# Kernel tuning notes

Measured on AMD Instinct MI355X. Metric: run time of the kernel, lower is better.

## Reference

```python
import jax, jax.numpy as jnp
import numpy as np

B, S, D = 2, 2048, 1024
H, A = 16, 64  # num_heads, attention_dim


def setup_inputs() -> dict:
    key = jax.random.key(0)
    ks = jax.random.split(key, 9)
    sd = D ** -0.5
    so = (H * A) ** -0.5
    return {
        "x": jax.random.normal(ks[0], (B, S, D), dtype=jnp.float32),
        "Wq": jax.random.normal(ks[1], (D, H * A), dtype=jnp.float32) * sd,
        "bq": jnp.zeros((H * A,), dtype=jnp.float32),
        "Wk": jax.random.normal(ks[2], (D, H * A), dtype=jnp.float32) * sd,
        "bk": jnp.zeros((H * A,), dtype=jnp.float32),
        "Wv": jax.random.normal(ks[3], (D, H * A), dtype=jnp.float32) * sd,
        "bv": jnp.zeros((H * A,), dtype=jnp.float32),
        "Wo": jax.random.normal(ks[4], (H * A, D), dtype=jnp.float32) * so,
        "bo": jnp.zeros((D,), dtype=jnp.float32),
    }


def reference(x, Wq, bq, Wk, bk, Wv, bv, Wo, bo):
    b, s, _ = x.shape
    # project and split heads: [b, s, H, A]
    q = (x @ Wq + bq).reshape(b, s, H, A)
    k = (x @ Wk + bk).reshape(b, s, H, A)
    v = (x @ Wv + bv).reshape(b, s, H, A)
    # scores [b, H, s, s]
    scores = jnp.einsum("bqhd,bkhd->bhqk", q, k) / jnp.sqrt(jnp.float32(A))
    weights = jax.nn.softmax(scores, axis=-1)
    attended = jnp.einsum("bhqk,bkhd->bqhd", weights, v).reshape(b, s, H * A)
    return attended @ Wo + bo
```

## Files before the change

### kernel.cpp

```cpp
#include <hip/hip_runtime.h>
#include <hip/hip_bf16.h>

typedef __attribute__((ext_vector_type(8))) short bf16x8;
typedef __attribute__((ext_vector_type(4))) float f32x4;

#define LOG2E 1.44269504088896f

extern "C" __device__ float __ocml_native_exp2_f32(float);

__device__ __forceinline__ unsigned short f2bf(float f) {
    union { float f; unsigned int u; } v; v.f = f;
    unsigned int r = v.u + 0x7FFF + ((v.u >> 16) & 1);
    return (unsigned short)(r >> 16);
}

__device__ __forceinline__ unsigned int pk_bf16(float lo, float hi) {
    unsigned int r;
    asm("v_cvt_pk_bf16_f32 %0, %1, %2" : "=v"(r) : "v"(lo), "v"(hi));
    return r;
}

typedef __attribute__((address_space(3))) unsigned int lds_uint;
typedef __attribute__((address_space(1))) const unsigned int glob_uint;
__device__ __forceinline__ void gl2lds16(const void* g, void* l) {
    __builtin_amdgcn_global_load_lds((glob_uint*)g, (lds_uint*)l, 16, 0, 0);
}

__global__ __launch_bounds__(256) void cvt_bf16(const float* __restrict__ in,
                                                unsigned int* __restrict__ out, int n4) {
    int i = blockIdx.x * 256 + threadIdx.x;
    if (i >= n4) return;
    float4 v = ((const float4*)in)[i];
    uint2 o;
    o.x = pk_bf16(v.x, v.y);
    o.y = pk_bf16(v.z, v.w);
    ((uint2*)out)[i] = o;
}

__global__ __launch_bounds__(256) void transpose4_bf16(
    const float* __restrict__ w0, const float* __restrict__ w1,
    const float* __restrict__ w2, const float* __restrict__ w3,
    unsigned short* __restrict__ o0, unsigned short* __restrict__ o1,
    unsigned short* __restrict__ o2, unsigned short* __restrict__ o3) {
    const int z = blockIdx.z;
    const float* in = (z == 0) ? w0 : (z == 1) ? w1 : (z == 2) ? w2 : w3;
    unsigned short* out = (z == 0) ? o0 : (z == 1) ? o1 : (z == 2) ? o2 : o3;
    __shared__ float t[32][33];
    int tx = threadIdx.x & 31, ty = threadIdx.x >> 5;
    int r0 = blockIdx.y * 32, c0 = blockIdx.x * 32;
    for (int i = 0; i < 32; i += 8)
        t[ty + i][tx] = in[(size_t)(r0 + ty + i) * 1024 + c0 + tx];
    __syncthreads();
    for (int i = 0; i < 32; i += 8)
        out[(size_t)(c0 + ty + i) * 1024 + r0 + tx] = f2bf(t[tx][ty + i]);
}

__device__ __forceinline__ void gemm_core(const short* __restrict__ A,
                                          const short* __restrict__ BT,
                                          int K, int bm0, int bn0,
                                          short* As, short* Bs, f32x4 acc[4][4]) {
    const int tid = threadIdx.x;
    const int lane = tid & 63;
    const int w = tid >> 6;
    const int wr0 = (w >> 1) * 64;
    const int wc0 = (w & 1) * 64;
    const int l15 = lane & 15, quad = lane >> 4;
    const int sr = lane >> 2;
    const int slog = (lane & 3) ^ (sr & 3);

    for (int i = 0; i < 4; i++)
        for (int j = 0; j < 4; j++) acc[i][j] = (f32x4)0.f;

    for (int k0 = 0; k0 < K; k0 += 32) {
        for (int i = 0; i < 4; i++) {
            int c = w * 4 + i;
            if (c < 8)
                gl2lds16(A + (size_t)(bm0 + c * 16 + sr) * K + k0 + slog * 8,
                         As + c * 512);
            else
                gl2lds16(BT + (size_t)(bn0 + (c - 8) * 16 + sr) * K + k0 + slog * 8,
                         Bs + (c - 8) * 512);
        }
        __syncthreads();
        const int ph = (quad ^ (l15 & 3)) * 8;
        bf16x8 af[4], bfr[4];
        for (int im = 0; im < 4; im++)
            af[im] = *(const bf16x8*)&As[(wr0 + im * 16 + l15) * 32 + ph];
        for (int in = 0; in < 4; in++)
            bfr[in] = *(const bf16x8*)&Bs[(wc0 + in * 16 + l15) * 32 + ph];
        for (int im = 0; im < 4; im++)
            for (int in = 0; in < 4; in++)
                acc[im][in] = __builtin_amdgcn_mfma_f32_16x16x32_bf16(af[im], bfr[in], acc[im][in], 0, 0, 0);
        __syncthreads();
    }
}

__global__ __launch_bounds__(256) void gemm_qkv(
    const short* __restrict__ xb,
    const short* __restrict__ wqT, const short* __restrict__ wkT, const short* __restrict__ wvT,
    const float* __restrict__ bq, const float* __restrict__ bk, const float* __restrict__ bv,
    unsigned short* __restrict__ qb, unsigned short* __restrict__ kb, unsigned short* __restrict__ vTb) {
    __shared__ short As[4096], Bs[4096];
    const int z = blockIdx.z;
    const short* Amat = (z == 2) ? wvT : xb;
    const short* Bmat = (z == 0) ? wqT : (z == 1) ? wkT : xb;
    const float* bias = (z == 0) ? bq : (z == 1) ? bk : bv;
    const float scl = (z == 0) ? 0.125f * LOG2E : 1.f;
    const int bm0 = (z == 2) ? blockIdx.y * 128 : blockIdx.x * 128;
    const int bn0 = (z == 2) ? blockIdx.x * 128 : blockIdx.y * 128;
    f32x4 acc[4][4];
    gemm_core(Amat, Bmat, 1024, bm0, bn0, As, Bs, acc);
    const int lane = threadIdx.x & 63, w = threadIdx.x >> 6;
    const int wr0 = (w >> 1) * 64, wc0 = (w & 1) * 64, l15 = lane & 15, quad = lane >> 4;
    if (z == 2) {
        for (int im = 0; im < 4; im++)
            for (int in = 0; in < 4; in++)
                for (int r = 0; r < 4; r++) {
                    int rowa = bm0 + wr0 + im * 16 + quad * 4 + r;
                    int colg = bn0 + wc0 + in * 16 + l15;
                    unsigned short ov = f2bf(acc[im][in][r] + bias[rowa]);
                    int b = colg >> 11, s = colg & 2047;
                    vTb[(size_t)b * 2097152 + (size_t)rowa * 2048 + s] = ov;
                }
    } else {
        for (int im = 0; im < 4; im++)
            for (int in = 0; in < 4; in++)
                for (int r = 0; r < 4; r++) {
                    int rowg = bm0 + wr0 + im * 16 + quad * 4 + r;
                    int colg = bn0 + wc0 + in * 16 + l15;
                    unsigned short ov = f2bf((acc[im][in][r] + bias[colg]) * scl);
                    int b = rowg >> 11, s = rowg & 2047;
                    int h = colg >> 6, a = colg & 63;
                    int bh = b * 16 + h;
                    if (z == 0) qb[((size_t)bh * 2048 + s) * 64 + a] = ov;
                    else        kb[((size_t)bh * 2048 + s) * 64 + a] = ov;
                }
    }
}

__global__ __launch_bounds__(512, 2) void gemm_out(
    const short* __restrict__ att, const short* __restrict__ woT,
    const float* __restrict__ bo, float* __restrict__ out) {
    __shared__ short As[4096], Bs[4096];
    const int bm0 = blockIdx.x * 128, bn0 = blockIdx.y * 128;
    const int tid = threadIdx.x, lane = tid & 63, w = tid >> 6;
    const int wr0 = (w >> 1) * 32, wc0 = (w & 1) * 64;
    const int l15 = lane & 15, quad = lane >> 4;
    const int sr = lane >> 2;
    const int slog = (lane & 3) ^ (sr & 3);

    f32x4 acc[2][4];
    for (int i = 0; i < 2; i++)
        for (int j = 0; j < 4; j++) acc[i][j] = (f32x4)0.f;

    for (int k0 = 0; k0 < 1024; k0 += 32) {
        for (int i = 0; i < 2; i++) {
            int c = w * 2 + i;
            if (c < 8)
                gl2lds16(att + (size_t)(bm0 + c * 16 + sr) * 1024 + k0 + slog * 8,
                         As + c * 512);
            else
                gl2lds16(woT + (size_t)(bn0 + (c - 8) * 16 + sr) * 1024 + k0 + slog * 8,
                         Bs + (c - 8) * 512);
        }
        __syncthreads();
        const int ph = (quad ^ (l15 & 3)) * 8;
        bf16x8 af[2], bfr[4];
        for (int im = 0; im < 2; im++)
            af[im] = *(const bf16x8*)&As[(wr0 + im * 16 + l15) * 32 + ph];
        for (int in = 0; in < 4; in++)
            bfr[in] = *(const bf16x8*)&Bs[(wc0 + in * 16 + l15) * 32 + ph];
        for (int im = 0; im < 2; im++)
            for (int in = 0; in < 4; in++)
                acc[im][in] = __builtin_amdgcn_mfma_f32_16x16x32_bf16(af[im], bfr[in], acc[im][in], 0, 0, 0);
        __syncthreads();
    }
    for (int im = 0; im < 2; im++)
        for (int in = 0; in < 4; in++)
            for (int r = 0; r < 4; r++) {
                int rowg = bm0 + wr0 + im * 16 + quad * 4 + r;
                int colg = bn0 + wc0 + in * 16 + l15;
                out[(size_t)rowg * 1024 + colg] = acc[im][in][r] + bo[colg];
            }
}

__global__ __launch_bounds__(256, 2) void flash_attn(
    const unsigned short* __restrict__ qb, const unsigned short* __restrict__ kb,
    const unsigned short* __restrict__ vTb, unsigned short* __restrict__ att) {
    __shared__ short QP[9216];
    __shared__ short Ks[2][4096];
    __shared__ short Vs[2][4096];
    const int tid = threadIdx.x, lane = tid & 63, w = tid >> 6;
    const int l15 = lane & 15, quad = lane >> 4;
    const int q0 = blockIdx.x * 128;
    const int bh = blockIdx.y;
    const size_t qkbase = (size_t)bh * 2048 * 64;
    const size_t vbase = (size_t)bh * 64 * 2048;
    const int sr = lane >> 3;
    const int slog = (lane & 7) ^ sr;
    const int l7 = l15 & 7;

    for (int i = 0; i < 8; i++) {
        int c = w * 8 + i;
        if (c < 16)
            gl2lds16(qb + qkbase + (size_t)(q0 + c * 8 + sr) * 64 + slog * 8, QP + c * 512);
        else if (c < 24)
            gl2lds16(kb + qkbase + (size_t)((c - 16) * 8 + sr) * 64 + slog * 8,
                     Ks[0] + (c - 16) * 512);
        else
            gl2lds16(vTb + vbase + (size_t)((c - 24) * 8 + sr) * 2048 + slog * 8,
                     Vs[0] + (c - 24) * 512);
    }
    __syncthreads();

    const int wq0 = w * 32;
    const int c0 = (quad ^ l7) * 8, c1 = c0 ^ 32;
    const int fb = l15 * 64;
    bf16x8 aqA0 = *(const bf16x8*)&QP[(wq0 + l15) * 64 + c0];
    bf16x8 aqB0 = *(const bf16x8*)&QP[(wq0 + l15) * 64 + c1];
    bf16x8 aqA1 = *(const bf16x8*)&QP[(wq0 + 16 + l15) * 64 + c0];
    bf16x8 aqB1 = *(const bf16x8*)&QP[(wq0 + 16 + l15) * 64 + c1];
    __syncthreads();

    f32x4 o[4][2];
    for (int dt = 0; dt < 4; dt++)
        for (int rt = 0; rt < 2; rt++) o[dt][rt] = (f32x4)0.f;
    f32x4 ls0 = (f32x4)0.f, ls1 = (f32x4)0.f;

    short* Pw = QP + w * 2304;
    short* Pst = Pw + l15 * 72 + quad * 4;
    const short* Prd = Pw + l15 * 72 + quad * 8;

    const unsigned short* sgp;
    int sgcall, sgtile;
    short *sb0, *sb1;
    if (w < 2) {
        sgp = kb + qkbase + (size_t)(64 + w * 32 + sr) * 64 + slog * 8;
        sgcall = 512;
        sgtile = 4096;
        sb0 = Ks[0] + w * 2048; sb1 = Ks[1] + w * 2048;
    } else {
        sgp = vTb + vbase + (size_t)((w - 2) * 32 + sr) * 2048 + 64 + slog * 8;
        sgcall = 16384;
        sgtile = 64;
        sb0 = Vs[0] + (w - 2) * 2048; sb1 = Vs[1] + (w - 2) * 2048;
    }

    auto step = [&](const short* Kb, const short* Vb, bool stage,
                    const unsigned short* sg, short* sd) {
        if (stage) {
#pragma unroll
            for (int i = 0; i < 4; i++)
                gl2lds16(sg + (size_t)i * sgcall, sd + i * 512);
        }
        f32x4 sc[4][2];
#pragma unroll
        for (int t = 0; t < 4; t++) {
            bf16x8 ak = *(const bf16x8*)(Kb + fb + c0 + t * 1024);
            sc[t][0] = __builtin_amdgcn_mfma_f32_16x16x32_bf16(ak, aqA0, (f32x4)0.f, 0, 0, 0);
            sc[t][1] = __builtin_amdgcn_mfma_f32_16x16x32_bf16(ak, aqA1, (f32x4)0.f, 0, 0, 0);
        }
#pragma unroll
        for (int t = 0; t < 4; t++) {
            bf16x8 ak = *(const bf16x8*)(Kb + fb + c1 + t * 1024);
            sc[t][0] = __builtin_amdgcn_mfma_f32_16x16x32_bf16(ak, aqB0, sc[t][0], 0, 0, 0);
            sc[t][1] = __builtin_amdgcn_mfma_f32_16x16x32_bf16(ak, aqB1, sc[t][1], 0, 0, 0);
        }
#pragma unroll
        for (int t = 0; t < 4; t++) {
#pragma unroll
            for (int r = 0; r < 4; r++) {
                sc[t][0][r] = __ocml_native_exp2_f32(sc[t][0][r]);
                sc[t][1][r] = __ocml_native_exp2_f32(sc[t][1][r]);
            }
            ls0 += sc[t][0];
            ls1 += sc[t][1];
            uint2 pk0, pk1;
            pk0.x = pk_bf16(sc[t][0][0], sc[t][0][1]);
            pk0.y = pk_bf16(sc[t][0][2], sc[t][0][3]);
            pk1.x = pk_bf16(sc[t][1][0], sc[t][1][1]);
            pk1.y = pk_bf16(sc[t][1][2], sc[t][1][3]);
            *(uint2*)(Pst + t * 16) = pk0;
            *(uint2*)(Pst + 1152 + t * 16) = pk1;
        }
#pragma unroll
        for (int t2 = 0; t2 < 2; t2++) {
            bf16x8 bp0 = *(const bf16x8*)(Prd + t2 * 32);
            bf16x8 bp1 = *(const bf16x8*)(Prd + 1152 + t2 * 32);
            const int cc = t2 ? c1 : c0;
#pragma unroll
            for (int dt = 0; dt < 4; dt++) {
                bf16x8 av = *(const bf16x8*)(Vb + fb + cc + dt * 1024);
                o[dt][0] = __builtin_amdgcn_mfma_f32_16x16x32_bf16(av, bp0, o[dt][0], 0, 0, 0);
                o[dt][1] = __builtin_amdgcn_mfma_f32_16x16x32_bf16(av, bp1, o[dt][1], 0, 0, 0);
            }
        }
        __syncthreads();
    };

    for (int kv0 = 0; kv0 < 2048; kv0 += 128) {
        step(Ks[0], Vs[0], true, sgp, sb1);
        sgp += sgtile;
        step(Ks[1], Vs[1], kv0 + 128 < 2048, sgp, sb0);
        sgp += sgtile;
    }

    const int b = bh >> 4, h = bh & 15;
#pragma unroll
    for (int rt = 0; rt < 2; rt++) {
        f32x4 ls = rt ? ls1 : ls0;
        float l = (ls[0] + ls[1]) + (ls[2] + ls[3]);
        l += __shfl_xor(l, 16);
        l += __shfl_xor(l, 32);
        float inv = 1.f / l;
        int s = q0 + wq0 + rt * 16 + l15;
        for (int dt = 0; dt < 4; dt++) {
            uint2 pk;
            pk.x = pk_bf16(o[dt][rt][0] * inv, o[dt][rt][1] * inv);
            pk.y = pk_bf16(o[dt][rt][2] * inv, o[dt][rt][3] * inv);
            int col = h * 64 + dt * 16 + quad * 4;
            *(uint2*)&att[((size_t)b * 2048 + s) * 1024 + col] = pk;
        }
    }
}

extern "C" void kernel_launch(void* const* d_in, const int* in_sizes, int n_in,
                              void* d_out, int out_size, void* d_ws, size_t ws_size,
                              hipStream_t stream) {
    const float* x  = (const float*)d_in[0];
    const float* Wq = (const float*)d_in[1];
    const float* bq = (const float*)d_in[2];
    const float* Wk = (const float*)d_in[3];
    const float* bk = (const float*)d_in[4];
    const float* Wv = (const float*)d_in[5];
    const float* bv = (const float*)d_in[6];
    const float* Wo = (const float*)d_in[7];
    const float* bo = (const float*)d_in[8];
    float* out = (float*)d_out;

    short* ws  = (short*)d_ws;
    short* xb  = ws;
    short* wqT = ws + 4 * 1024 * 1024;
    short* wkT = wqT + 1024 * 1024;
    short* wvT = wkT + 1024 * 1024;
    short* woT = wvT + 1024 * 1024;
    short* qb  = woT + 1024 * 1024;
    short* kb  = qb + 4 * 1024 * 1024;
    short* vTb = kb + 4 * 1024 * 1024;
    short* att = vTb + 4 * 1024 * 1024;

    cvt_bf16<<<4096, 256, 0, stream>>>(x, (unsigned int*)xb, 1024 * 1024);
    transpose4_bf16<<<dim3(32, 32, 4), 256, 0, stream>>>(
        Wq, Wk, Wv, Wo,
        (unsigned short*)wqT, (unsigned short*)wkT,
        (unsigned short*)wvT, (unsigned short*)woT);
    gemm_qkv<<<dim3(32, 8, 3), 256, 0, stream>>>(xb, wqT, wkT, wvT, bq, bk, bv,
                                                 (unsigned short*)qb, (unsigned short*)kb,
                                                 (unsigned short*)vTb);
    flash_attn<<<dim3(16, 32), 256, 0, stream>>>((const unsigned short*)qb,
                                                 (const unsigned short*)kb,
                                                 (const unsigned short*)vTb,
                                                 (unsigned short*)att);
    gemm_out<<<dim3(32, 8), 512, 0, stream>>>(att, woT, bo, out);
}
```

Before: 208.7 us.

## Load K/V fragments directly into registers, dropping LDS staging and barriers

```diff
diff --git a/kernel.cpp b/kernel.cpp
--- a/kernel.cpp
+++ b/kernel.cpp
@@ -187,133 +187,93 @@
 __global__ __launch_bounds__(256, 2) void flash_attn(
     const unsigned short* __restrict__ qb, const unsigned short* __restrict__ kb,
     const unsigned short* __restrict__ vTb, unsigned short* __restrict__ att) {
-    __shared__ short QP[9216];
-    __shared__ short Ks[2][4096];
-    __shared__ short Vs[2][4096];
+    __shared__ short Ps[4][32 * 40];
     const int tid = threadIdx.x, lane = tid & 63, w = tid >> 6;
     const int l15 = lane & 15, quad = lane >> 4;
     const int q0 = blockIdx.x * 128;
     const int bh = blockIdx.y;
-    const size_t qkbase = (size_t)bh * 2048 * 64;
-    const size_t vbase = (size_t)bh * 64 * 2048;
-    const int sr = lane >> 3;
-    const int slog = (lane & 7) ^ sr;
-    const int l7 = l15 & 7;
-
-    for (int i = 0; i < 8; i++) {
-        int c = w * 8 + i;
-        if (c < 16)
-            gl2lds16(qb + qkbase + (size_t)(q0 + c * 8 + sr) * 64 + slog * 8, QP + c * 512);
-        else if (c < 24)
-            gl2lds16(kb + qkbase + (size_t)((c - 16) * 8 + sr) * 64 + slog * 8,
-                     Ks[0] + (c - 16) * 512);
-        else
-            gl2lds16(vTb + vbase + (size_t)((c - 24) * 8 + sr) * 2048 + slog * 8,
-                     Vs[0] + (c - 24) * 512);
-    }
-    __syncthreads();
-
-    const int wq0 = w * 32;
-    const int c0 = (quad ^ l7) * 8, c1 = c0 ^ 32;
-    const int fb = l15 * 64;
-    bf16x8 aqA0 = *(const bf16x8*)&QP[(wq0 + l15) * 64 + c0];
-    bf16x8 aqB0 = *(const bf16x8*)&QP[(wq0 + l15) * 64 + c1];
-    bf16x8 aqA1 = *(const bf16x8*)&QP[(wq0 + 16 + l15) * 64 + c0];
-    bf16x8 aqB1 = *(const bf16x8*)&QP[(wq0 + 16 + l15) * 64 + c1];
-    __syncthreads();
+    const size_t base = (size_t)bh * 131072;
+
+    const unsigned short* qptr = qb + base + (size_t)(q0 + w * 32 + l15) * 64 + quad * 8;
+    bf16x8 aq[2][2];
+#pragma unroll
+    for (int rt = 0; rt < 2; rt++)
+#pragma unroll
+        for (int ks = 0; ks < 2; ks++)
+            aq[rt][ks] = *(const bf16x8*)(qptr + rt * 1024 + ks * 32);
+
+    const unsigned short* kptr = kb + base + (size_t)l15 * 64 + quad * 8;
+    const unsigned short* vptr = vTb + base + (size_t)l15 * 2048 + quad * 8;
 
     f32x4 o[4][2];
     for (int dt = 0; dt < 4; dt++)
         for (int rt = 0; rt < 2; rt++) o[dt][rt] = (f32x4)0.f;
-    f32x4 ls0 = (f32x4)0.f, ls1 = (f32x4)0.f;
-
-    short* Pw = QP + w * 2304;
-    short* Pst = Pw + l15 * 72 + quad * 4;
-    const short* Prd = Pw + l15 * 72 + quad * 8;
-
-    const unsigned short* sgp;
-    int sgcall, sgtile;
-    short *sb0, *sb1;
-    if (w < 2) {
-        sgp = kb + qkbase + (size_t)(64 + w * 32 + sr) * 64 + slog * 8;
-        sgcall = 512;
-        sgtile = 4096;
-        sb0 = Ks[0] + w * 2048; sb1 = Ks[1] + w * 2048;
-    } else {
-        sgp = vTb + vbase + (size_t)((w - 2) * 32 + sr) * 2048 + 64 + slog * 8;
-        sgcall = 16384;
-        sgtile = 64;
-        sb0 = Vs[0] + (w - 2) * 2048; sb1 = Vs[1] + (w - 2) * 2048;
-    }
-
-    auto step = [&](const short* Kb, const short* Vb, bool stage,
-                    const unsigned short* sg, short* sd) {
-        if (stage) {
-#pragma unroll
-            for (int i = 0; i < 4; i++)
-                gl2lds16(sg + (size_t)i * sgcall, sd + i * 512);
+    f32x4 ls[2] = {(f32x4)0.f, (f32x4)0.f};
+
+    short* Pw = Ps[w];
+    short* Pst = Pw + l15 * 40 + quad * 4;
+    const short* Prd = Pw + l15 * 40 + quad * 8;
+
+    bf16x8 kfA[4], kfB[4], vfA[4], vfB[4];
+    auto ldK = [&](int kv, bf16x8* kf) {
+#pragma unroll
+        for (int t = 0; t < 2; t++)
+#pragma unroll
+            for (int ks = 0; ks < 2; ks++)
+                kf[t * 2 + ks] = *(const bf16x8*)(kptr + (size_t)(kv + t * 16) * 64 + ks * 32);
+    };
+    auto ldV = [&](int kv, bf16x8* vf) {
+#pragma unroll
+        for (int dt = 0; dt < 4; dt++)
+            vf[dt] = *(const bf16x8*)(vptr + (size_t)dt * 32768 + kv);
+    };
+
+    auto step = [&](const bf16x8* kf, const bf16x8* vf) {
+        f32x4 sc[2][2];
+#pragma unroll
+        for (int t = 0; t < 2; t++)
+#pragma unroll
+            for (int rt = 0; rt < 2; rt++) {
+                sc[t][rt] = __builtin_amdgcn_mfma_f32_16x16x32_bf16(kf[t * 2], aq[rt][0], (f32x4)0.f, 0, 0, 0);
+                sc[t][rt] = __builtin_amdgcn_mfma_f32_16x16x32_bf16(kf[t * 2 + 1], aq[rt][1], sc[t][rt], 0, 0, 0);
+            }
+#pragma unroll
+        for (int t = 0; t < 2; t++)
+#pragma unroll
+            for (int rt = 0; rt < 2; rt++) {
+#pragma unroll
+                for (int r = 0; r < 4; r++) sc[t][rt][r] = __ocml_native_exp2_f32(sc[t][rt][r]);
+                ls[rt] += sc[t][rt];
+                uint2 pk;
+                pk.x = pk_bf16(sc[t][rt][0], sc[t][rt][1]);
+                pk.y = pk_bf16(sc[t][rt][2], sc[t][rt][3]);
+                *(uint2*)(Pst + rt * 640 + t * 16) = pk;
+            }
+        bf16x8 bp0 = *(const bf16x8*)(Prd);
+        bf16x8 bp1 = *(const bf16x8*)(Prd + 640);
+#pragma unroll
+        for (int dt = 0; dt < 4; dt++) {
+            o[dt][0] = __builtin_amdgcn_mfma_f32_16x16x32_bf16(vf[dt], bp0, o[dt][0], 0, 0, 0);
+            o[dt][1] = __builtin_amdgcn_mfma_f32_16x16x32_bf16(vf[dt], bp1, o[dt][1], 0, 0, 0);
         }
-        f32x4 sc[4][2];
-#pragma unroll
-        for (int t = 0; t < 4; t++) {
-            bf16x8 ak = *(const bf16x8*)(Kb + fb + c0 + t * 1024);
-            sc[t][0] = __builtin_amdgcn_mfma_f32_16x16x32_bf16(ak, aqA0, (f32x4)0.f, 0, 0, 0);
-            sc[t][1] = __builtin_amdgcn_mfma_f32_16x16x32_bf16(ak, aqA1, (f32x4)0.f, 0, 0, 0);
-        }
-#pragma unroll
-        for (int t = 0; t < 4; t++) {
-            bf16x8 ak = *(const bf16x8*)(Kb + fb + c1 + t * 1024);
-            sc[t][0] = __builtin_amdgcn_mfma_f32_16x16x32_bf16(ak, aqB0, sc[t][0], 0, 0, 0);
-            sc[t][1] = __builtin_amdgcn_mfma_f32_16x16x32_bf16(ak, aqB1, sc[t][1], 0, 0, 0);
-        }
-#pragma unroll
-        for (int t = 0; t < 4; t++) {
-#pragma unroll
-            for (int r = 0; r < 4; r++) {
-                sc[t][0][r] = __ocml_native_exp2_f32(sc[t][0][r]);
-                sc[t][1][r] = __ocml_native_exp2_f32(sc[t][1][r]);
-            }
-            ls0 += sc[t][0];
-            ls1 += sc[t][1];
-            uint2 pk0, pk1;
-            pk0.x = pk_bf16(sc[t][0][0], sc[t][0][1]);
-            pk0.y = pk_bf16(sc[t][0][2], sc[t][0][3]);
-            pk1.x = pk_bf16(sc[t][1][0], sc[t][1][1]);
-            pk1.y = pk_bf16(sc[t][1][2], sc[t][1][3]);
-            *(uint2*)(Pst + t * 16) = pk0;
-            *(uint2*)(Pst + 1152 + t * 16) = pk1;
-        }
-#pragma unroll
-        for (int t2 = 0; t2 < 2; t2++) {
-            bf16x8 bp0 = *(const bf16x8*)(Prd + t2 * 32);
-            bf16x8 bp1 = *(const bf16x8*)(Prd + 1152 + t2 * 32);
-            const int cc = t2 ? c1 : c0;
-#pragma unroll
-            for (int dt = 0; dt < 4; dt++) {
-                bf16x8 av = *(const bf16x8*)(Vb + fb + cc + dt * 1024);
-                o[dt][0] = __builtin_amdgcn_mfma_f32_16x16x32_bf16(av, bp0, o[dt][0], 0, 0, 0);
-                o[dt][1] = __builtin_amdgcn_mfma_f32_16x16x32_bf16(av, bp1, o[dt][1], 0, 0, 0);
-            }
-        }
-        __syncthreads();
     };
 
-    for (int kv0 = 0; kv0 < 2048; kv0 += 128) {
-        step(Ks[0], Vs[0], true, sgp, sb1);
-        sgp += sgtile;
-        step(Ks[1], Vs[1], kv0 + 128 < 2048, sgp, sb0);
-        sgp += sgtile;
+    ldK(0, kfA); ldV(0, vfA);
+    for (int kv0 = 0; kv0 < 2048; kv0 += 64) {
+        ldK(kv0 + 32, kfB); ldV(kv0 + 32, vfB);
+        step(kfA, vfA);
+        ldK(kv0 + 64, kfA); ldV(kv0 + 64, vfA);
+        step(kfB, vfB);
     }
 
     const int b = bh >> 4, h = bh & 15;
 #pragma unroll
     for (int rt = 0; rt < 2; rt++) {
-        f32x4 ls = rt ? ls1 : ls0;
-        float l = (ls[0] + ls[1]) + (ls[2] + ls[3]);
+        float l = (ls[rt][0] + ls[rt][1]) + (ls[rt][2] + ls[rt][3]);
         l += __shfl_xor(l, 16);
         l += __shfl_xor(l, 32);
         float inv = 1.f / l;
-        int s = q0 + wq0 + rt * 16 + l15;
+        int s = q0 + w * 32 + rt * 16 + l15;
         for (int dt = 0; dt < 4; dt++) {
             uint2 pk;
             pk.x = pk_bf16(o[dt][rt][0] * inv, o[dt][rt][1] * inv);
```

After: 279.6 us. 34.0% more time.

## Split attention over KV halves with a merge pass; reuse shared GEMM core for output

Applied to the files above, without the earlier changes.

```diff
diff --git a/kernel.cpp b/kernel.cpp
--- a/kernel.cpp
+++ b/kernel.cpp
@@ -1,5 +1,6 @@
 #include <hip/hip_runtime.h>
 #include <hip/hip_bf16.h>
+#include <hip/hip_fp16.h>
 
 typedef __attribute__((ext_vector_type(8))) short bf16x8;
 typedef __attribute__((ext_vector_type(4))) float f32x4;
@@ -17,6 +18,12 @@
 __device__ __forceinline__ unsigned int pk_bf16(float lo, float hi) {
     unsigned int r;
     asm("v_cvt_pk_bf16_f32 %0, %1, %2" : "=v"(r) : "v"(lo), "v"(hi));
+    return r;
+}
+
+__device__ __forceinline__ unsigned int pk_f16(float lo, float hi) {
+    unsigned int r;
+    asm("v_cvt_pkrtz_f16_f32 %0, %1, %2" : "=v"(r) : "v"(lo), "v"(hi));
     return r;
 }
 
@@ -138,44 +145,16 @@
     }
 }
 
-__global__ __launch_bounds__(512, 2) void gemm_out(
+__global__ __launch_bounds__(256) void gemm_out(
     const short* __restrict__ att, const short* __restrict__ woT,
     const float* __restrict__ bo, float* __restrict__ out) {
     __shared__ short As[4096], Bs[4096];
     const int bm0 = blockIdx.x * 128, bn0 = blockIdx.y * 128;
-    const int tid = threadIdx.x, lane = tid & 63, w = tid >> 6;
-    const int wr0 = (w >> 1) * 32, wc0 = (w & 1) * 64;
-    const int l15 = lane & 15, quad = lane >> 4;
-    const int sr = lane >> 2;
-    const int slog = (lane & 3) ^ (sr & 3);
-
-    f32x4 acc[2][4];
-    for (int i = 0; i < 2; i++)
-        for (int j = 0; j < 4; j++) acc[i][j] = (f32x4)0.f;
-
-    for (int k0 = 0; k0 < 1024; k0 += 32) {
-        for (int i = 0; i < 2; i++) {
-            int c = w * 2 + i;
-            if (c < 8)
-                gl2lds16(att + (size_t)(bm0 + c * 16 + sr) * 1024 + k0 + slog * 8,
-                         As + c * 512);
-            else
-                gl2lds16(woT + (size_t)(bn0 + (c - 8) * 16 + sr) * 1024 + k0 + slog * 8,
-                         Bs + (c - 8) * 512);
-        }
-        __syncthreads();
-        const int ph = (quad ^ (l15 & 3)) * 8;
-        bf16x8 af[2], bfr[4];
-        for (int im = 0; im < 2; im++)
-            af[im] = *(const bf16x8*)&As[(wr0 + im * 16 + l15) * 32 + ph];
-        for (int in = 0; in < 4; in++)
-            bfr[in] = *(const bf16x8*)&Bs[(wc0 + in * 16 + l15) * 32 + ph];
-        for (int im = 0; im < 2; im++)
-            for (int in = 0; in < 4; in++)
-                acc[im][in] = __builtin_amdgcn_mfma_f32_16x16x32_bf16(af[im], bfr[in], acc[im][in], 0, 0, 0);
-        __syncthreads();
-    }
-    for (int im = 0; im < 2; im++)
+    f32x4 acc[4][4];
+    gemm_core(att, woT, 1024, bm0, bn0, As, Bs, acc);
+    const int lane = threadIdx.x & 63, w = threadIdx.x >> 6;
+    const int wr0 = (w >> 1) * 64, wc0 = (w & 1) * 64, l15 = lane & 15, quad = lane >> 4;
+    for (int im = 0; im < 4; im++)
         for (int in = 0; in < 4; in++)
             for (int r = 0; r < 4; r++) {
                 int rowg = bm0 + wr0 + im * 16 + quad * 4 + r;
@@ -184,9 +163,11 @@
             }
 }
 
-__global__ __launch_bounds__(256, 2) void flash_attn(
+__global__ __launch_bounds__(256, 2) void flash_partial(
     const unsigned short* __restrict__ qb, const unsigned short* __restrict__ kb,
-    const unsigned short* __restrict__ vTb, unsigned short* __restrict__ att) {
+    const unsigned short* __restrict__ vTb,
+    unsigned short* __restrict__ op0, unsigned short* __restrict__ op1,
+    float* __restrict__ lp) {
     __shared__ short QP[9216];
     __shared__ short Ks[2][4096];
     __shared__ short Vs[2][4096];
@@ -194,8 +175,10 @@
     const int l15 = lane & 15, quad = lane >> 4;
     const int q0 = blockIdx.x * 128;
     const int bh = blockIdx.y;
-    const size_t qkbase = (size_t)bh * 2048 * 64;
-    const size_t vbase = (size_t)bh * 64 * 2048;
+    const int half = blockIdx.z;
+    const unsigned short* kbh  = kb  + (size_t)bh * 131072 + (size_t)half * 65536;
+    const unsigned short* vTbh = vTb + (size_t)bh * 131072 + half * 1024;
+    const unsigned short* qbb  = qb  + (size_t)bh * 131072;
     const int sr = lane >> 3;
     const int slog = (lane & 7) ^ sr;
     const int l7 = l15 & 7;
@@ -203,12 +186,12 @@
     for (int i = 0; i < 8; i++) {
         int c = w * 8 + i;
         if (c < 16)
-            gl2lds16(qb + qkbase + (size_t)(q0 + c * 8 + sr) * 64 + slog * 8, QP + c * 512);
+            gl2lds16(qbb + (size_t)(q0 + c * 8 + sr) * 64 + slog * 8, QP + c * 512);
         else if (c < 24)
-            gl2lds16(kb + qkbase + (size_t)((c - 16) * 8 + sr) * 64 + slog * 8,
+            gl2lds16(kbh + (size_t)((c - 16) * 8 + sr) * 64 + slog * 8,
                      Ks[0] + (c - 16) * 512);
         else
-            gl2lds16(vTb + vbase + (size_t)((c - 24) * 8 + sr) * 2048 + slog * 8,
+            gl2lds16(vTbh + (size_t)((c - 24) * 8 + sr) * 2048 + slog * 8,
                      Vs[0] + (c - 24) * 512);
     }
     __syncthreads();
@@ -235,12 +218,12 @@
     int sgcall, sgtile;
     short *sb0, *sb1;
     if (w < 2) {
-        sgp = kb + qkbase + (size_t)(64 + w * 32 + sr) * 64 + slog * 8;
+        sgp = kbh + (size_t)(64 + w * 32 + sr) * 64 + slog * 8;
         sgcall = 512;
         sgtile = 4096;
         sb0 = Ks[0] + w * 2048; sb1 = Ks[1] + w * 2048;
     } else {
-        sgp = vTb + vbase + (size_t)((w - 2) * 32 + sr) * 2048 + 64 + slog * 8;
+        sgp = vTbh + (size_t)((w - 2) * 32 + sr) * 2048 + 64 + slog * 8;
         sgcall = 16384;
         sgtile = 64;
         sb0 = Vs[0] + (w - 2) * 2048; sb1 = Vs[1] + (w - 2) * 2048;
@@ -298,30 +281,53 @@
         __syncthreads();
     };
 
-    for (int kv0 = 0; kv0 < 2048; kv0 += 128) {
+    for (int kv0 = 0; kv0 < 1024; kv0 += 128) {
         step(Ks[0], Vs[0], true, sgp, sb1);
         sgp += sgtile;
-        step(Ks[1], Vs[1], kv0 + 128 < 2048, sgp, sb0);
+        step(Ks[1], Vs[1], kv0 + 128 < 1024, sgp, sb0);
         sgp += sgtile;
     }
 
     const int b = bh >> 4, h = bh & 15;
+    unsigned short* op = half ? op1 : op0;
 #pragma unroll
     for (int rt = 0; rt < 2; rt++) {
         f32x4 ls = rt ? ls1 : ls0;
         float l = (ls[0] + ls[1]) + (ls[2] + ls[3]);
         l += __shfl_xor(l, 16);
         l += __shfl_xor(l, 32);
-        float inv = 1.f / l;
         int s = q0 + wq0 + rt * 16 + l15;
+        if (quad == 0) lp[(size_t)half * 65536 + bh * 2048 + s] = l;
         for (int dt = 0; dt < 4; dt++) {
             uint2 pk;
-            pk.x = pk_bf16(o[dt][rt][0] * inv, o[dt][rt][1] * inv);
-            pk.y = pk_bf16(o[dt][rt][2] * inv, o[dt][rt][3] * inv);
+            pk.x = pk_f16(o[dt][rt][0], o[dt][rt][1]);
+            pk.y = pk_f16(o[dt][rt][2], o[dt][rt][3]);
             int col = h * 64 + dt * 16 + quad * 4;
-            *(uint2*)&att[((size_t)b * 2048 + s) * 1024 + col] = pk;
-        }
-    }
+            *(uint2*)&op[((size_t)b * 2048 + s) * 1024 + col] = pk;
+        }
+    }
+}
+
+__global__ __launch_bounds__(256) void merge_att(
+    const unsigned short* __restrict__ p0, const float* __restrict__ l0,
+    const float* __restrict__ l1, unsigned short* __restrict__ att) {
+    int i4 = blockIdx.x * 256 + threadIdx.x;
+    int i = i4 * 4;
+    int row = i >> 10;
+    int h = (i & 1023) >> 6;
+    int b = row >> 11, s = row & 2047;
+    int bhs = (b * 16 + h) * 2048 + s;
+    float inv = 1.f / (l0[bhs] + l1[bhs]);
+    ushort4 a = *(const ushort4*)&p0[i];
+    ushort4 c = *(const ushort4*)&att[i];
+    float x0 = __half2float(__ushort_as_half(a.x)) + __half2float(__ushort_as_half(c.x));
+    float x1 = __half2float(__ushort_as_half(a.y)) + __half2float(__ushort_as_half(c.y));
+    float x2 = __half2float(__ushort_as_half(a.z)) + __half2float(__ushort_as_half(c.z));
+    float x3 = __half2float(__ushort_as_half(a.w)) + __half2float(__ushort_as_half(c.w));
+    uint2 pk;
+    pk.x = pk_bf16(x0 * inv, x1 * inv);
+    pk.y = pk_bf16(x2 * inv, x3 * inv);
+    *(uint2*)&att[i] = pk;
 }
 
 extern "C" void kernel_launch(void* const* d_in, const int* in_sizes, int n_in,
@@ -348,6 +354,9 @@
     short* kb  = qb + 4 * 1024 * 1024;
     short* vTb = kb + 4 * 1024 * 1024;
     short* att = vTb + 4 * 1024 * 1024;
+    unsigned short* op0 = (unsigned short*)xb;
+    unsigned short* op1 = (unsigned short*)att;
+    float* lp = (float*)wkT;
 
     cvt_bf16<<<4096, 256, 0, stream>>>(x, (unsigned int*)xb, 1024 * 1024);
     transpose4_bf16<<<dim3(32, 32, 4), 256, 0, stream>>>(
@@ -357,9 +366,9 @@
     gemm_qkv<<<dim3(32, 8, 3), 256, 0, stream>>>(xb, wqT, wkT, wvT, bq, bk, bv,
                                                  (unsigned short*)qb, (unsigned short*)kb,
                                                  (unsigned short*)vTb);
-    flash_attn<<<dim3(16, 32), 256, 0, stream>>>((const unsigned short*)qb,
-                                                 (const unsigned short*)kb,
-                                                 (const unsigned short*)vTb,
-                                                 (unsigned short*)att);
-    gemm_out<<<dim3(32, 8), 512, 0, stream>>>(att, woT, bo, out);
-}
+    flash_partial<<<dim3(16, 32, 2), 256, 0, stream>>>(
+        (const unsigned short*)qb, (const unsigned short*)kb,
+        (const unsigned short*)vTb, op0, op1, lp);
+    merge_att<<<4096, 256, 0, stream>>>(op0, lp, lp + 65536, (unsigned short*)att);
+    gemm_out<<<dim3(32, 8), 256, 0, stream>>>(att, woT, bo, out);
+}
```

After: 210.6 us. About the same (+0.9%).
